# Kernel optimization log

Measured on AMD Instinct MI355X. Metric: run time of the kernel, lower is better.

Reference implementation:

```python
import jax, jax.numpy as jnp
import numpy as np

EPS = 1e-6

def setup_inputs() -> dict:
    key = jax.random.key(0)
    k1, k2 = jax.random.split(key)
    b, seq, d = 4, 512, 64
    x = jax.random.normal(k1, (b, seq, d, d), dtype=jnp.float32)
    # diagonal decay rates in (0, 1): realistic SSM decay, positive like the clamped param
    A = jax.random.uniform(k2, (d,), dtype=jnp.float32)
    return {"x": x, "A": A}

def reference(x, A):
    b, seq, d, _ = x.shape
    log_A = jnp.log(jnp.clip(A, EPS))                      # (d,)
    # cumsum over seq of the (constant-in-time) log decay, as in the original
    cs_A = jnp.cumsum(jnp.broadcast_to(log_A, (seq, d)), axis=0)  # (seq, d)
    log_M = cs_A[:, None, :] - cs_A[None, :, :]            # (t, j, d)
    idx = jnp.arange(seq)
    mask = idx[:, None] >= idx[None, :]                    # causal: t >= j
    M = jnp.where(mask[:, :, None], jnp.exp(log_M), 0.0)   # (t, j, d)
    # A is batch-independent, so M is shared across batch (same math as the original)
    out = jnp.einsum('tjr,bjrc->btrc', M, x)               # (b, seq, d, d)
    return out
```

## Files before the change

### kernel.cpp

```cpp
#include <hip/hip_runtime.h>


#define B_    4
#define SEQ_  512
#define D_    64
#define CH_   8
#define NCH_  (SEQ_ / CH_)
#define NCQ_  (D_ / 4)
#define NTHR_ (NCH_ * NCQ_)

typedef float f32x4 __attribute__((ext_vector_type(4)));

__global__ __launch_bounds__(NTHR_, 1) void ssm_scan_kernel(
    const float* __restrict__ x, const float* __restrict__ A,
    float* __restrict__ out)
{
    __shared__ float4 Elds[NCH_][NCQ_];

    const int blk = blockIdx.x;
    const int bi  = blk >> 6;
    const int r   = blk & 63;
    const int tid = threadIdx.x;
    const int ch  = tid >> 4;
    const int cq  = tid & 15;

    const float a = fmaxf(A[r], 1e-6f);

    const int j0 = ch * CH_;
    const size_t base = ((size_t)(bi * SEQ_ + j0) * D_ + r) * D_ + cq * 4;
    const float4* xp = (const float4*)(x + base);
    f32x4*        op = (f32x4*)(out + base);
    const int jstride4 = (D_ * D_) / 4;

    float4 loc[CH_];
    float s0 = 0.f, s1 = 0.f, s2 = 0.f, s3 = 0.f;
    #pragma unroll
    for (int t = 0; t < CH_; ++t) {
        float4 v = xp[(size_t)t * jstride4];
        s0 = fmaf(s0, a, v.x);
        s1 = fmaf(s1, a, v.y);
        s2 = fmaf(s2, a, v.z);
        s3 = fmaf(s3, a, v.w);
        loc[t] = make_float4(s0, s1, s2, s3);
    }

    #pragma unroll
    for (int t = 0; t < CH_; ++t) {
        asm volatile("" : "+v"(loc[t].x), "+v"(loc[t].y),
                         "+v"(loc[t].z), "+v"(loc[t].w));
    }

    if (ch < NCH_ - 1) {
        Elds[ch][cq] = make_float4(s0, s1, s2, s3);
    }
    __syncthreads();

    float a2 = a * a, a4 = a2 * a2, aL = a4 * a4;

    float c0 = 0.f, c1 = 0.f, c2 = 0.f, c3 = 0.f;
    for (int cp = 0; cp < ch; ++cp) {
        float4 e = Elds[cp][cq];
        c0 = fmaf(c0, aL, e.x);
        c1 = fmaf(c1, aL, e.y);
        c2 = fmaf(c2, aL, e.z);
        c3 = fmaf(c3, aL, e.w);
    }

    float p = a;
    #pragma unroll
    for (int t = 0; t < CH_; ++t) {
        float4 l = loc[t];
        f32x4 o;
        o.x = fmaf(c0, p, l.x);
        o.y = fmaf(c1, p, l.y);
        o.z = fmaf(c2, p, l.z);
        o.w = fmaf(c3, p, l.w);
        __builtin_nontemporal_store(o, &op[(size_t)t * jstride4]);
        p *= a;
    }
}

extern "C" void kernel_launch(void* const* d_in, const int* in_sizes, int n_in,
                              void* d_out, int out_size, void* d_ws, size_t ws_size,
                              hipStream_t stream) {
    const float* x   = (const float*)d_in[0];
    const float* A   = (const float*)d_in[1];
    float*       out = (float*)d_out;

    dim3 grid(B_ * D_);
    dim3 block(NTHR_);
    hipLaunchKernelGGL(ssm_scan_kernel, grid, block, 0, stream, x, A, out);
}
```

Measured before the change: 81.86 us.

## Replace serial cross-chunk carry loop with wavefront shuffle parallel scan

The serial loop over up to 63 preceding chunk end-states in LDS is replaced by a log-depth Hillis-Steele scan. Each of 16 waves scans the 64 chunk totals for one column quad using __shfl_up, with decay powers squared each step. A padded LDS array avoids bank conflicts on the transposed access. This removes the O(NCH) per-thread LDS loop, which was worst for the last chunks, at the cost of an extra barrier and shuffle traffic.

```diff
diff --git a/kernel.cpp b/kernel.cpp
--- a/kernel.cpp
+++ b/kernel.cpp
@@ -8,6 +8,7 @@
 #define NCH_  (SEQ_ / CH_)
 #define NCQ_  (D_ / 4)
 #define NTHR_ (NCH_ * NCQ_)
+#define PAD_  (NCQ_ + 1)
 
 typedef float f32x4 __attribute__((ext_vector_type(4)));
 
@@ -15,7 +16,7 @@
     const float* __restrict__ x, const float* __restrict__ A,
     float* __restrict__ out)
 {
-    __shared__ float4 Elds[NCH_][NCQ_];
+    __shared__ float4 Epad[NCH_][PAD_];
 
     const int blk = blockIdx.x;
     const int bi  = blk >> 6;
@@ -50,20 +51,39 @@
                          "+v"(loc[t].z), "+v"(loc[t].w));
     }
 
-    if (ch < NCH_ - 1) {
-        Elds[ch][cq] = make_float4(s0, s1, s2, s3);
+    Epad[ch][cq] = make_float4(s0, s1, s2, s3);
+    __syncthreads();
+
+    const float a2 = a * a, a4 = a2 * a2, aL = a4 * a4;
+
+    {
+        const int w = tid >> 6;
+        const int m = tid & 63;
+        float4 v = Epad[m][w];
+        float aw = aL;
+        #pragma unroll
+        for (int s = 0; s < 6; ++s) {
+            const int d = 1 << s;
+            float ux = __shfl_up(v.x, d, 64);
+            float uy = __shfl_up(v.y, d, 64);
+            float uz = __shfl_up(v.z, d, 64);
+            float uw = __shfl_up(v.w, d, 64);
+            if (m >= d) {
+                v.x = fmaf(aw, ux, v.x);
+                v.y = fmaf(aw, uy, v.y);
+                v.z = fmaf(aw, uz, v.z);
+                v.w = fmaf(aw, uw, v.w);
+            }
+            aw *= aw;
+        }
+        Epad[m][w] = v;
     }
     __syncthreads();
 
-    float a2 = a * a, a4 = a2 * a2, aL = a4 * a4;
-
     float c0 = 0.f, c1 = 0.f, c2 = 0.f, c3 = 0.f;
-    for (int cp = 0; cp < ch; ++cp) {
-        float4 e = Elds[cp][cq];
-        c0 = fmaf(c0, aL, e.x);
-        c1 = fmaf(c1, aL, e.y);
-        c2 = fmaf(c2, aL, e.z);
-        c3 = fmaf(c3, aL, e.w);
+    if (ch > 0) {
+        float4 c4 = Epad[ch - 1][cq];
+        c0 = c4.x; c1 = c4.y; c2 = c4.z; c3 = c4.w;
     }
 
     float p = a;
```

Measured after the change: 83.22 us. About the same (+1.7%).
